# Kernel optimization log

Measured on AMD Instinct MI355X. Metric: run time of the kernel, lower is better.

The kernel has to match this reference:

```python
import jax, jax.numpy as jnp
import numpy as np

DIM = 320
NUM_HEADS = 5
HEAD_DIM = DIM // NUM_HEADS  # 64
SCALE = HEAD_DIM ** -0.5


def setup_inputs() -> dict:
    key = jax.random.key(0)
    k1, k2, k3, k4 = jax.random.split(key, 4)
    B, N, C = 8, 2048, DIM
    x = jax.random.normal(k1, (B, N, C), dtype=jnp.float32)
    # nn.Linear(dim, dim*3, bias=False): weight [3*dim, dim]
    w_qkv = jax.random.normal(k2, (3 * C, C), dtype=jnp.float32) * (C ** -0.5)
    # nn.Linear(dim, dim): weight [dim, dim], bias [dim]
    w_proj = jax.random.normal(k3, (C, C), dtype=jnp.float32) * (C ** -0.5)
    b_proj = jax.random.normal(k4, (C,), dtype=jnp.float32) * 0.01
    return {"x": x, "w_qkv": w_qkv, "w_proj": w_proj, "b_proj": b_proj}


def reference(x, w_qkv, w_proj, b_proj):
    B, N, C = x.shape
    H, D = NUM_HEADS, HEAD_DIM
    # qkv projection: [B, N, 3C] -> [3, B, H, N, D]
    qkv = jnp.einsum('bnc,kc->bnk', x, w_qkv)
    qkv = qkv.reshape(B, N, 3, H, D).transpose(2, 0, 3, 1, 4)
    q, k, v = qkv[0], qkv[1], qkv[2]
    # full attention matrix [B, H, N, N] (retained by original module)
    attn = jnp.einsum('bhnd,bhmd->bhnm', q, k) * SCALE
    attn = jax.nn.softmax(attn, axis=-1)
    # attn_drop p=0 -> identity (eval/deterministic)
    out = jnp.einsum('bhnm,bhmd->bhnd', attn, v)
    out = out.transpose(0, 2, 1, 3).reshape(B, N, C)
    out = jnp.einsum('bnc,oc->bno', out, w_proj) + b_proj
    # proj_drop p=0 -> identity
    return out
```

## Files before the change

kernel.cpp:

```cpp
#include <hip/hip_runtime.h>
#include <hip/hip_bf16.h>


typedef __attribute__((ext_vector_type(8))) short bf16x8;
typedef __attribute__((ext_vector_type(4))) float f32x4;

#define MFMA(a, b, c) __builtin_amdgcn_mfma_f32_16x16x32_bf16((a), (b), (c), 0, 0, 0)

#define QSCALE 0.18033688322643216f

static __device__ inline bf16x8 ld8(const __hip_bfloat16* p) {
    return *reinterpret_cast<const bf16x8*>(p);
}

static __device__ inline unsigned short bfbits(float v) {
    unsigned int u = __builtin_bit_cast(unsigned int, v);
    u += 0x7FFFu + ((u >> 16) & 1u);
    return (unsigned short)(u >> 16);
}

static __device__ inline unsigned int cvtpk(float lo, float hi) {
    unsigned int r;
    asm("v_cvt_pk_bf16_f32 %0, %1, %2" : "=v"(r) : "v"(lo), "v"(hi));
    return r;
}

static __device__ inline void gload_lds16(const __hip_bfloat16* g, __hip_bfloat16* l) {
    __builtin_amdgcn_global_load_lds(
        (const __attribute__((address_space(1))) void*)g,
        (__attribute__((address_space(3))) void*)l, 16, 0, 0);
}

static __device__ inline bf16x8 cvt8(const float* src) {
    float4 a = *reinterpret_cast<const float4*>(src);
    float4 b = *reinterpret_cast<const float4*>(src + 4);
    bf16x8 v;
    v[0] = (short)bfbits(a.x); v[1] = (short)bfbits(a.y);
    v[2] = (short)bfbits(a.z); v[3] = (short)bfbits(a.w);
    v[4] = (short)bfbits(b.x); v[5] = (short)bfbits(b.y);
    v[6] = (short)bfbits(b.z); v[7] = (short)bfbits(b.w);
    return v;
}

__global__ __launch_bounds__(256)
void cvt_x(const float* __restrict__ x, __hip_bfloat16* __restrict__ xb)
{
    const size_t tid = (size_t)blockIdx.x * blockDim.x + threadIdx.x;
    const size_t stride = (size_t)gridDim.x * blockDim.x;
    const float4* x4 = (const float4*)x;
    ushort4* xb4 = (ushort4*)xb;
    for (size_t i = tid; i < 1310720u; i += stride) {
        float4 v = x4[i];
        ushort4 u;
        u.x = bfbits(v.x); u.y = bfbits(v.y);
        u.z = bfbits(v.z); u.w = bfbits(v.w);
        xb4[i] = u;
    }
}

__global__ __launch_bounds__(256)
void qkv_kernel(const __hip_bfloat16* __restrict__ xb,
                const float* __restrict__ w,
                __hip_bfloat16* __restrict__ qout,
                __hip_bfloat16* __restrict__ kp,
                __hip_bfloat16* __restrict__ vp)
{
    __shared__ __align__(16) __hip_bfloat16 As[128 * 72];
    __shared__ __align__(16) __hip_bfloat16 Bs[64 * 72];

    const int tid  = threadIdx.x;
    const int wv   = tid >> 6;
    const int lane = tid & 63;
    const int quad = lane >> 4;
    const int col  = lane & 15;

    const int id  = blockIdx.x;
    const int xcd = id & 7;
    const int r9  = id >> 3;
    const int m0  = (xcd * 16 + r9 / 15) * 128;
    const int ny  = r9 % 15;
    const int n0  = ny * 64;

    f32x4 acc[2][4];
#pragma unroll
    for (int i = 0; i < 2; ++i)
#pragma unroll
        for (int j = 0; j < 4; ++j) acc[i][j] = (f32x4){0.f, 0.f, 0.f, 0.f};

    for (int k0 = 0; k0 < 320; k0 += 64) {
        __syncthreads();
#pragma unroll
        for (int i = 0; i < 4; ++i) {
            int ch = tid + i * 256;
            int r = ch >> 3, sg = ch & 7;
            *reinterpret_cast<float4*>(&As[r * 72 + sg * 8]) =
                *reinterpret_cast<const float4*>(&xb[(m0 + r) * 320 + k0 + sg * 8]);
        }
#pragma unroll
        for (int i = 0; i < 2; ++i) {
            int ch = tid + i * 256;
            int r = ch >> 3, sg = ch & 7;
            *reinterpret_cast<bf16x8*>(&Bs[r * 72 + sg * 8]) =
                cvt8(&w[(n0 + r) * 320 + k0 + sg * 8]);
        }
        __syncthreads();

#pragma unroll
        for (int hf = 0; hf < 2; ++hf) {
            bf16x8 a0 = ld8(&As[(wv * 32 + col) * 72 + hf * 32 + quad * 8]);
            bf16x8 a1 = ld8(&As[(wv * 32 + 16 + col) * 72 + hf * 32 + quad * 8]);
#pragma unroll
            for (int nt = 0; nt < 4; ++nt) {
                bf16x8 b = ld8(&Bs[(nt * 16 + col) * 72 + hf * 32 + quad * 8]);
                acc[0][nt] = MFMA(a0, b, acc[0][nt]);
                acc[1][nt] = MFMA(a1, b, acc[1][nt]);
            }
        }
    }

    const int s = ny / 5;
    const int h = ny % 5;
    unsigned short* qo = (unsigned short*)qout;
    unsigned short* ko = (unsigned short*)kp;
    unsigned short* vo = (unsigned short*)vp;
#pragma unroll
    for (int mt = 0; mt < 2; ++mt) {
#pragma unroll
        for (int nt = 0; nt < 4; ++nt) {
#pragma unroll
            for (int r = 0; r < 4; ++r) {
                int m = m0 + wv * 32 + mt * 16 + quad * 4 + r;
                int d = nt * 16 + col;
                int b = m >> 11, n = m & 2047;
                int bh = b * 5 + h;
                float val = acc[mt][nt][r];
                if (s == 0) {
                    qo[((size_t)bh * 2048 + n) * 64 + d] = bfbits(val * QSCALE);
                } else if (s == 1) {
                    int p = n >> 6, nn = n & 63;
                    size_t a = ((size_t)(bh * 32 + p) * 8 + (d >> 5) * 4 + (nn >> 4)) * 512
                             + (((d >> 3) & 3) * 16 + (nn & 15)) * 8 + (d & 7);
                    ko[a] = bfbits(val);
                } else {
                    int p = n >> 6;
                    size_t a = ((size_t)(bh * 32 + p) * 8 + ((n >> 5) & 1) * 4 + (d >> 4)) * 512
                             + (((n >> 3) & 3) * 16 + (d & 15)) * 8 + (n & 7);
                    vo[a] = bfbits(val);
                }
            }
        }
    }
}

__global__ __launch_bounds__(256)
void attn_kernel(const __hip_bfloat16* __restrict__ Q,
                 const __hip_bfloat16* __restrict__ Kp,
                 const __hip_bfloat16* __restrict__ Vp,
                 __hip_bfloat16* __restrict__ A2)
{
    __shared__ __align__(16) __hip_bfloat16 KV[16384];
    __shared__ __align__(16) unsigned char psraw[18432];

    const int tid  = threadIdx.x;
    const int wv   = tid >> 6;
    const int lane = tid & 63;
    const int quad = lane >> 4;
    const int col  = lane & 15;

    const int id  = blockIdx.x;
    const int xcd = id & 7;
    const int j   = id >> 3;
    const int bh  = xcd * 5 + (j >> 4);
    const int q0w = (j & 15) * 128 + wv * 32;
    const int b   = bh / 5, h = bh % 5;

    char* psb = (char*)psraw + wv * 4608;
    char* ps_w = psb + col * 144 + quad * 8;
    const __hip_bfloat16* ps_r =
        (const __hip_bfloat16*)psb + col * 72 + quad * 8;

    const __hip_bfloat16* kg = Kp + (size_t)bh * 131072;
    const __hip_bfloat16* vg = Vp + (size_t)bh * 131072;
    const __hip_bfloat16* Qh = Q + (size_t)bh * 131072;

    bf16x8 qf[2][2];
#pragma unroll
    for (int mt = 0; mt < 2; ++mt)
#pragma unroll
        for (int hf = 0; hf < 2; ++hf)
            qf[mt][hf] = ld8(&Qh[(q0w + mt * 16 + col) * 64 + hf * 32 + quad * 8]);

    f32x4 lp[2];
    f32x4 o[2][4];
#pragma unroll
    for (int mt = 0; mt < 2; ++mt) {
        lp[mt] = (f32x4){0.f, 0.f, 0.f, 0.f};
#pragma unroll
        for (int dt = 0; dt < 4; ++dt) o[mt][dt] = (f32x4){0.f, 0.f, 0.f, 0.f};
    }

    auto stage = [&](int t, int c) {
        const __hip_bfloat16* kp_ = kg + (size_t)t * 4096 + wv * 1024 + lane * 8;
        const __hip_bfloat16* vp_ = vg + (size_t)t * 4096 + wv * 1024 + lane * 8;
        __hip_bfloat16* kl = &KV[c * 4096 + wv * 1024];
        __hip_bfloat16* vl = &KV[8192 + c * 4096 + wv * 1024];
        gload_lds16(kp_, kl);
        gload_lds16(kp_ + 512, kl + 512);
        gload_lds16(vp_, vl);
        gload_lds16(vp_ + 512, vl + 512);
    };

    stage(0, 0);

    for (int t = 0; t < 32; ++t) {
        const int c = t & 1;
        asm volatile("s_waitcnt vmcnt(0)" ::: "memory");
        __builtin_amdgcn_s_barrier();
        stage((t < 31) ? t + 1 : 31, c ^ 1);

        const __hip_bfloat16* kb = &KV[c * 4096];
        const __hip_bfloat16* vb = &KV[8192 + c * 4096];

        f32x4 s[2][4];
#pragma unroll
        for (int nt = 0; nt < 4; ++nt) {
            bf16x8 k0 = ld8(kb + nt * 512 + lane * 8);
            bf16x8 k1 = ld8(kb + (4 + nt) * 512 + lane * 8);
#pragma unroll
            for (int mt = 0; mt < 2; ++mt) {
                f32x4 z = (f32x4){0.f, 0.f, 0.f, 0.f};
                z = MFMA(k0, qf[mt][0], z);
                z = MFMA(k1, qf[mt][1], z);
                s[mt][nt] = z;
            }
        }

#pragma unroll
        for (int mt = 0; mt < 2; ++mt)
#pragma unroll
            for (int nt = 0; nt < 4; ++nt) {
                f32x4 pv;
#pragma unroll
                for (int r = 0; r < 4; ++r)
                    pv[r] = __builtin_amdgcn_exp2f(s[mt][nt][r]);
                lp[mt] += pv;
                uint2 wpk;
                wpk.x = cvtpk(pv[0], pv[1]);
                wpk.y = cvtpk(pv[2], pv[3]);
                *reinterpret_cast<uint2*>(ps_w + mt * 2304 + nt * 32) = wpk;
            }
        __asm__ volatile("s_waitcnt lgkmcnt(0)" ::: "memory");

#pragma unroll
        for (int mt = 0; mt < 2; ++mt)
#pragma unroll
            for (int kk = 0; kk < 2; ++kk) {
                bf16x8 pf = ld8(ps_r + mt * 1152 + kk * 32);
#pragma unroll
                for (int dt = 0; dt < 4; ++dt) {
                    bf16x8 va = ld8(vb + (kk * 4 + dt) * 512 + lane * 8);
                    o[mt][dt] = MFMA(pf, va, o[mt][dt]);
                }
            }
    }

    float lsum[2];
#pragma unroll
    for (int mt = 0; mt < 2; ++mt) {
        float v = lp[mt][0] + lp[mt][1] + lp[mt][2] + lp[mt][3];
        v += __shfl_xor(v, 16, 64);
        v += __shfl_xor(v, 32, 64);
        lsum[mt] = v;
    }

    float* lw = (float*)psb;
    if (quad == 0) {
#pragma unroll
        for (int mt = 0; mt < 2; ++mt)
            lw[mt * 16 + col] = lsum[mt];
    }
    __asm__ volatile("s_waitcnt lgkmcnt(0)" ::: "memory");

    unsigned short* a2o = (unsigned short*)A2;
#pragma unroll
    for (int mt = 0; mt < 2; ++mt) {
#pragma unroll
        for (int r = 0; r < 4; ++r) {
            int row = mt * 16 + quad * 4 + r;
            float inv = 1.0f / lw[row];
            int grow = q0w + row;
#pragma unroll
            for (int dt = 0; dt < 4; ++dt) {
                int d = dt * 16 + col;
                a2o[((size_t)(b * 2048 + grow)) * 320 + h * 64 + d] =
                    bfbits(o[mt][dt][r] * inv);
            }
        }
    }
}

__global__ __launch_bounds__(256)
void proj_kernel(const __hip_bfloat16* __restrict__ a2,
                 const float* __restrict__ w,
                 const float* __restrict__ bias,
                 float* __restrict__ out)
{
    __shared__ __align__(16) __hip_bfloat16 As[128 * 72];
    __shared__ __align__(16) __hip_bfloat16 Bs[64 * 72];

    const int tid  = threadIdx.x;
    const int wv   = tid >> 6;
    const int lane = tid & 63;
    const int quad = lane >> 4;
    const int col  = lane & 15;

    const int id  = blockIdx.x;
    const int xcd = id & 7;
    const int r9  = id >> 3;
    const int m0  = (xcd * 16 + r9 / 5) * 128;
    const int n0  = (r9 % 5) * 64;

    f32x4 acc[2][4];
#pragma unroll
    for (int i = 0; i < 2; ++i)
#pragma unroll
        for (int j = 0; j < 4; ++j) acc[i][j] = (f32x4){0.f, 0.f, 0.f, 0.f};

    for (int k0 = 0; k0 < 320; k0 += 64) {
        __syncthreads();
#pragma unroll
        for (int i = 0; i < 4; ++i) {
            int ch = tid + i * 256;
            int r = ch >> 3, sg = ch & 7;
            *reinterpret_cast<float4*>(&As[r * 72 + sg * 8]) =
                *reinterpret_cast<const float4*>(&a2[(m0 + r) * 320 + k0 + sg * 8]);
        }
#pragma unroll
        for (int i = 0; i < 2; ++i) {
            int ch = tid + i * 256;
            int r = ch >> 3, sg = ch & 7;
            *reinterpret_cast<bf16x8*>(&Bs[r * 72 + sg * 8]) =
                cvt8(&w[(n0 + r) * 320 + k0 + sg * 8]);
        }
        __syncthreads();

#pragma unroll
        for (int hf = 0; hf < 2; ++hf) {
            bf16x8 a0 = ld8(&As[(wv * 32 + col) * 72 + hf * 32 + quad * 8]);
            bf16x8 a1 = ld8(&As[(wv * 32 + 16 + col) * 72 + hf * 32 + quad * 8]);
#pragma unroll
            for (int nt = 0; nt < 4; ++nt) {
                bf16x8 b = ld8(&Bs[(nt * 16 + col) * 72 + hf * 32 + quad * 8]);
                acc[0][nt] = MFMA(a0, b, acc[0][nt]);
                acc[1][nt] = MFMA(a1, b, acc[1][nt]);
            }
        }
    }

#pragma unroll
    for (int nt = 0; nt < 4; ++nt) {
        float bv = bias[n0 + nt * 16 + col];
#pragma unroll
        for (int mt = 0; mt < 2; ++mt) {
#pragma unroll
            for (int r = 0; r < 4; ++r) {
                int m = m0 + wv * 32 + mt * 16 + quad * 4 + r;
                out[(size_t)m * 320 + n0 + nt * 16 + col] = acc[mt][nt][r] + bv;
            }
        }
    }
}

extern "C" void kernel_launch(void* const* d_in, const int* in_sizes, int n_in,
                              void* d_out, int out_size, void* d_ws, size_t ws_size,
                              hipStream_t stream)
{
    const float* x      = (const float*)d_in[0];
    const float* w_qkv  = (const float*)d_in[1];
    const float* w_proj = (const float*)d_in[2];
    const float* b_proj = (const float*)d_in[3];
    float* out = (float*)d_out;

    const size_t NX = 5242880;
    __hip_bfloat16* xb = (__hip_bfloat16*)d_ws;
    __hip_bfloat16* q  = xb + NX;
    __hip_bfloat16* kp = q + NX;
    __hip_bfloat16* vp = kp + NX;
    __hip_bfloat16* a2 = xb;

    cvt_x<<<1024, 256, 0, stream>>>(x, xb);
    qkv_kernel<<<1920, 256, 0, stream>>>(xb, w_qkv, q, kp, vp);
    attn_kernel<<<640, 256, 0, stream>>>(q, kp, vp, a2);
    proj_kernel<<<640, 256, 0, stream>>>(a2, w_proj, b_proj, out);
}
```

Measured before the change: 175.0 us.

## Pre-convert weights to bf16 and double-buffer GEMM tiles via direct global-to-LDS loads

Weight matrices are now converted to bf16 once in a merged conversion kernel instead of per-tile fp32 loads and conversions inside the QKV and projection GEMMs. Both GEMMs switch to global_load_lds direct-to-LDS copies with an XOR swizzle in place of padding, and double-buffer the K tiles so the next tile loads while the current one is multiplied. This targets redundant weight conversion work and exposed load latency. It adds a larger workspace, twice the LDS per block, and a vmcnt(0) wait that may limit overlap.

```diff
diff --git a/kernel.cpp b/kernel.cpp
--- a/kernel.cpp
+++ b/kernel.cpp
@@ -31,42 +31,42 @@
         (__attribute__((address_space(3))) void*)l, 16, 0, 0);
 }
 
-static __device__ inline bf16x8 cvt8(const float* src) {
-    float4 a = *reinterpret_cast<const float4*>(src);
-    float4 b = *reinterpret_cast<const float4*>(src + 4);
-    bf16x8 v;
-    v[0] = (short)bfbits(a.x); v[1] = (short)bfbits(a.y);
-    v[2] = (short)bfbits(a.z); v[3] = (short)bfbits(a.w);
-    v[4] = (short)bfbits(b.x); v[5] = (short)bfbits(b.y);
-    v[6] = (short)bfbits(b.z); v[7] = (short)bfbits(b.w);
-    return v;
-}
-
 __global__ __launch_bounds__(256)
-void cvt_x(const float* __restrict__ x, __hip_bfloat16* __restrict__ xb)
+void cvt_all(const float* __restrict__ x,
+             const float* __restrict__ wq,
+             const float* __restrict__ wp,
+             __hip_bfloat16* __restrict__ xb,
+             __hip_bfloat16* __restrict__ wqb,
+             __hip_bfloat16* __restrict__ wpb)
 {
     const size_t tid = (size_t)blockIdx.x * blockDim.x + threadIdx.x;
     const size_t stride = (size_t)gridDim.x * blockDim.x;
-    const float4* x4 = (const float4*)x;
-    ushort4* xb4 = (ushort4*)xb;
-    for (size_t i = tid; i < 1310720u; i += stride) {
-        float4 v = x4[i];
+    for (size_t i = tid; i < 1413120u; i += stride) {
+        const float4* src; ushort4* dst; size_t j;
+        if (i < 1310720u) {
+            src = (const float4*)x;  dst = (ushort4*)xb;  j = i;
+        } else if (i < 1387520u) {
+            src = (const float4*)wq; dst = (ushort4*)wqb; j = i - 1310720u;
+        } else {
+            src = (const float4*)wp; dst = (ushort4*)wpb; j = i - 1387520u;
+        }
+        float4 v = src[j];
         ushort4 u;
         u.x = bfbits(v.x); u.y = bfbits(v.y);
         u.z = bfbits(v.z); u.w = bfbits(v.w);
-        xb4[i] = u;
+        dst[j] = u;
     }
 }
 
 __global__ __launch_bounds__(256)
 void qkv_kernel(const __hip_bfloat16* __restrict__ xb,
-                const float* __restrict__ w,
+                const __hip_bfloat16* __restrict__ wqb,
                 __hip_bfloat16* __restrict__ qout,
                 __hip_bfloat16* __restrict__ kp,
                 __hip_bfloat16* __restrict__ vp)
 {
-    __shared__ __align__(16) __hip_bfloat16 As[128 * 72];
-    __shared__ __align__(16) __hip_bfloat16 Bs[64 * 72];
+    __shared__ __align__(16) __hip_bfloat16 As[2 * 8192];
+    __shared__ __align__(16) __hip_bfloat16 Bs[2 * 4096];
 
     const int tid  = threadIdx.x;
     const int wv   = tid >> 6;
@@ -81,41 +81,52 @@
     const int ny  = r9 % 15;
     const int n0  = ny * 64;
 
-    f32x4 acc[2][4];
-#pragma unroll
-    for (int i = 0; i < 2; ++i)
-#pragma unroll
-        for (int j = 0; j < 4; ++j) acc[i][j] = (f32x4){0.f, 0.f, 0.f, 0.f};
-
-    for (int k0 = 0; k0 < 320; k0 += 64) {
-        __syncthreads();
+    auto stage = [&](int k0, int c) {
 #pragma unroll
         for (int i = 0; i < 4; ++i) {
             int ch = tid + i * 256;
             int r = ch >> 3, sg = ch & 7;
-            *reinterpret_cast<float4*>(&As[r * 72 + sg * 8]) =
-                *reinterpret_cast<const float4*>(&xb[(m0 + r) * 320 + k0 + sg * 8]);
+            gload_lds16(&xb[(size_t)(m0 + r) * 320 + k0 + ((sg ^ (r & 7)) * 8)],
+                        &As[c * 8192 + (i * 256 + wv * 64) * 8]);
         }
 #pragma unroll
         for (int i = 0; i < 2; ++i) {
             int ch = tid + i * 256;
             int r = ch >> 3, sg = ch & 7;
-            *reinterpret_cast<bf16x8*>(&Bs[r * 72 + sg * 8]) =
-                cvt8(&w[(n0 + r) * 320 + k0 + sg * 8]);
-        }
-        __syncthreads();
-
+            gload_lds16(&wqb[(size_t)(n0 + r) * 320 + k0 + ((sg ^ (r & 7)) * 8)],
+                        &Bs[c * 4096 + (i * 256 + wv * 64) * 8]);
+        }
+    };
+
+    f32x4 acc[2][4];
+#pragma unroll
+    for (int i = 0; i < 2; ++i)
+#pragma unroll
+        for (int j = 0; j < 4; ++j) acc[i][j] = (f32x4){0.f, 0.f, 0.f, 0.f};
+
+    stage(0, 0);
+
+    for (int kt = 0; kt < 5; ++kt) {
+        const int c = kt & 1;
+        asm volatile("s_waitcnt vmcnt(0)" ::: "memory");
+        __builtin_amdgcn_s_barrier();
+        if (kt < 4) stage((kt + 1) * 64, c ^ 1);
+
+        const __hip_bfloat16* Ab = &As[c * 8192];
+        const __hip_bfloat16* Bb = &Bs[c * 4096];
 #pragma unroll
         for (int hf = 0; hf < 2; ++hf) {
-            bf16x8 a0 = ld8(&As[(wv * 32 + col) * 72 + hf * 32 + quad * 8]);
-            bf16x8 a1 = ld8(&As[(wv * 32 + 16 + col) * 72 + hf * 32 + quad * 8]);
+            const int sw = ((hf * 4 + quad) ^ (col & 7)) * 8;
+            bf16x8 a0 = ld8(&Ab[(wv * 32 + col) * 64 + sw]);
+            bf16x8 a1 = ld8(&Ab[(wv * 32 + 16 + col) * 64 + sw]);
 #pragma unroll
             for (int nt = 0; nt < 4; ++nt) {
-                bf16x8 b = ld8(&Bs[(nt * 16 + col) * 72 + hf * 32 + quad * 8]);
+                bf16x8 b = ld8(&Bb[(nt * 16 + col) * 64 + sw]);
                 acc[0][nt] = MFMA(a0, b, acc[0][nt]);
                 acc[1][nt] = MFMA(a1, b, acc[1][nt]);
             }
         }
+        __builtin_amdgcn_s_barrier();
     }
 
     const int s = ny / 5;
@@ -301,12 +312,12 @@
 
 __global__ __launch_bounds__(256)
 void proj_kernel(const __hip_bfloat16* __restrict__ a2,
-                 const float* __restrict__ w,
+                 const __hip_bfloat16* __restrict__ wpb,
                  const float* __restrict__ bias,
                  float* __restrict__ out)
 {
-    __shared__ __align__(16) __hip_bfloat16 As[128 * 72];
-    __shared__ __align__(16) __hip_bfloat16 Bs[64 * 72];
+    __shared__ __align__(16) __hip_bfloat16 As[2 * 8192];
+    __shared__ __align__(16) __hip_bfloat16 Bs[2 * 4096];
 
     const int tid  = threadIdx.x;
     const int wv   = tid >> 6;
@@ -320,41 +331,52 @@
     const int m0  = (xcd * 16 + r9 / 5) * 128;
     const int n0  = (r9 % 5) * 64;
 
-    f32x4 acc[2][4];
-#pragma unroll
-    for (int i = 0; i < 2; ++i)
-#pragma unroll
-        for (int j = 0; j < 4; ++j) acc[i][j] = (f32x4){0.f, 0.f, 0.f, 0.f};
-
-    for (int k0 = 0; k0 < 320; k0 += 64) {
-        __syncthreads();
+    auto stage = [&](int k0, int c) {
 #pragma unroll
         for (int i = 0; i < 4; ++i) {
             int ch = tid + i * 256;
             int r = ch >> 3, sg = ch & 7;
-            *reinterpret_cast<float4*>(&As[r * 72 + sg * 8]) =
-                *reinterpret_cast<const float4*>(&a2[(m0 + r) * 320 + k0 + sg * 8]);
+            gload_lds16(&a2[(size_t)(m0 + r) * 320 + k0 + ((sg ^ (r & 7)) * 8)],
+                        &As[c * 8192 + (i * 256 + wv * 64) * 8]);
         }
 #pragma unroll
         for (int i = 0; i < 2; ++i) {
             int ch = tid + i * 256;
             int r = ch >> 3, sg = ch & 7;
-            *reinterpret_cast<bf16x8*>(&Bs[r * 72 + sg * 8]) =
-                cvt8(&w[(n0 + r) * 320 + k0 + sg * 8]);
-        }
-        __syncthreads();
-
+            gload_lds16(&wpb[(size_t)(n0 + r) * 320 + k0 + ((sg ^ (r & 7)) * 8)],
+                        &Bs[c * 4096 + (i * 256 + wv * 64) * 8]);
+        }
+    };
+
+    f32x4 acc[2][4];
+#pragma unroll
+    for (int i = 0; i < 2; ++i)
+#pragma unroll
+        for (int j = 0; j < 4; ++j) acc[i][j] = (f32x4){0.f, 0.f, 0.f, 0.f};
+
+    stage(0, 0);
+
+    for (int kt = 0; kt < 5; ++kt) {
+        const int c = kt & 1;
+        asm volatile("s_waitcnt vmcnt(0)" ::: "memory");
+        __builtin_amdgcn_s_barrier();
+        if (kt < 4) stage((kt + 1) * 64, c ^ 1);
+
+        const __hip_bfloat16* Ab = &As[c * 8192];
+        const __hip_bfloat16* Bb = &Bs[c * 4096];
 #pragma unroll
         for (int hf = 0; hf < 2; ++hf) {
-            bf16x8 a0 = ld8(&As[(wv * 32 + col) * 72 + hf * 32 + quad * 8]);
-            bf16x8 a1 = ld8(&As[(wv * 32 + 16 + col) * 72 + hf * 32 + quad * 8]);
+            const int sw = ((hf * 4 + quad) ^ (col & 7)) * 8;
+            bf16x8 a0 = ld8(&Ab[(wv * 32 + col) * 64 + sw]);
+            bf16x8 a1 = ld8(&Ab[(wv * 32 + 16 + col) * 64 + sw]);
 #pragma unroll
             for (int nt = 0; nt < 4; ++nt) {
-                bf16x8 b = ld8(&Bs[(nt * 16 + col) * 72 + hf * 32 + quad * 8]);
+                bf16x8 b = ld8(&Bb[(nt * 16 + col) * 64 + sw]);
                 acc[0][nt] = MFMA(a0, b, acc[0][nt]);
                 acc[1][nt] = MFMA(a1, b, acc[1][nt]);
             }
         }
+        __builtin_amdgcn_s_barrier();
     }
 
 #pragma unroll
@@ -382,14 +404,16 @@
     float* out = (float*)d_out;
 
     const size_t NX = 5242880;
-    __hip_bfloat16* xb = (__hip_bfloat16*)d_ws;
-    __hip_bfloat16* q  = xb + NX;
-    __hip_bfloat16* kp = q + NX;
-    __hip_bfloat16* vp = kp + NX;
-    __hip_bfloat16* a2 = xb;
-
-    cvt_x<<<1024, 256, 0, stream>>>(x, xb);
-    qkv_kernel<<<1920, 256, 0, stream>>>(xb, w_qkv, q, kp, vp);
+    __hip_bfloat16* xb  = (__hip_bfloat16*)d_ws;
+    __hip_bfloat16* q   = xb + NX;
+    __hip_bfloat16* kp  = q + NX;
+    __hip_bfloat16* vp  = kp + NX;
+    __hip_bfloat16* wqb = vp + NX;
+    __hip_bfloat16* wpb = wqb + 307200;
+    __hip_bfloat16* a2  = xb;
+
+    cvt_all<<<1024, 256, 0, stream>>>(x, w_qkv, w_proj, xb, wqb, wpb);
+    qkv_kernel<<<1920, 256, 0, stream>>>(xb, wqb, q, kp, vp);
     attn_kernel<<<640, 256, 0, stream>>>(q, kp, vp, a2);
-    proj_kernel<<<640, 256, 0, stream>>>(a2, w_proj, b_proj, out);
-}
+    proj_kernel<<<640, 256, 0, stream>>>(a2, wpb, b_proj, out);
+}
```

Measured after the change: 173.2 us. About the same (-1.0%).
